# Optimization experiments

Hardware: AMD Instinct MI355X
Metric: run time of the kernel (lower is better)

## Reference

```python
import jax, jax.numpy as jnp
import numpy as np

N = 100_000; E = 1_600_000; G = 64
D_IN = 128; POS = 16; HID = 32; HEADS = 4; OUT = 10
D0 = D_IN + POS; D1 = HID * HEADS
LRELU = 0.2; BN_EPS = 1e-5; DIV_W = 0.1


def setup_inputs() -> dict:
    key = jax.random.key(0)
    k = jax.random.split(key, 24)
    nrm = lambda ki, shape, s: jax.random.normal(ki, shape, dtype=jnp.float32) * s
    inp = {}
    inp["x"] = nrm(k[0], (N, D_IN), 1.0)
    inp["edge_index"] = jax.random.randint(k[1], (2, E), 0, N, dtype=jnp.int32)
    inp["batch"] = jnp.sort(jax.random.randint(k[2], (N,), 0, G, dtype=jnp.int32))
    inp["pos_w"] = nrm(k[3], (2, POS), 0.5)
    inp["pos_b"] = nrm(k[4], (POS,), 0.1)
    inp["w0"] = nrm(k[5], (D0, HEADS * HID), D0 ** -0.5)
    inp["asrc0"] = nrm(k[6], (HEADS, HID), HID ** -0.5)
    inp["adst0"] = nrm(k[7], (HEADS, HID), HID ** -0.5)
    inp["b0"] = nrm(k[8], (D1,), 0.1)
    inp["w1"] = nrm(k[9], (D1, HEADS * HID), D1 ** -0.5)
    inp["asrc1"] = nrm(k[10], (HEADS, HID), HID ** -0.5)
    inp["adst1"] = nrm(k[11], (HEADS, HID), HID ** -0.5)
    inp["b1"] = nrm(k[12], (D1,), 0.1)
    inp["bn_gamma"] = 1.0 + nrm(k[13], (2, D1), 0.1)
    inp["bn_beta"] = nrm(k[14], (2, D1), 0.1)
    inp["bn_mean"] = nrm(k[15], (2, D1), 0.1)
    inp["bn_var"] = jax.random.uniform(k[16], (2, D1), dtype=jnp.float32, minval=0.5, maxval=1.5)
    inp["proj"] = nrm(k[17], (2, HEADS, HID), HID ** -0.5)
    inp["res_w"] = nrm(k[18], (D1, D1), D1 ** -0.5)
    inp["res_b"] = nrm(k[19], (D1,), 0.1)
    inp["task_w"] = nrm(k[20], (D1, OUT), D1 ** -0.5)
    inp["task_b"] = nrm(k[21], (OUT,), 0.1)
    return inp


def _positions(batch):
    # vectorized version of the per-node Python loop: grid layout per graph
    counts = jnp.bincount(batch, length=G)               # nodes per graph
    starts = jnp.cumsum(counts) - counts                  # exclusive cumsum
    local = jnp.arange(N, dtype=counts.dtype) - starts[batch]
    grid = jnp.ceil(jnp.sqrt(counts.astype(jnp.float32))).astype(counts.dtype)
    g = jnp.maximum(grid[batch], 1)
    denom = jnp.maximum(g - 1, 1).astype(jnp.float32)
    row = (local // g).astype(jnp.float32)
    col = (local % g).astype(jnp.float32)
    return jnp.stack([row / denom, col / denom], axis=-1)  # (N, 2)


def _gat(x, src, dst, w, a_src, a_dst, bias):
    # PyG GATConv (v1) with self-loops already appended to src/dst
    n = x.shape[0]
    h = (x @ w).reshape(n, HEADS, HID)                     # (N, H, C)
    e = jax.nn.leaky_relu(jnp.sum(h * a_src, -1)[src] + jnp.sum(h * a_dst, -1)[dst], LRELU)  # (E+N, H)
    m = jax.lax.stop_gradient(jax.ops.segment_max(e, dst, num_segments=n))
    ex = jnp.exp(e - m[dst])
    alpha = ex / jax.ops.segment_sum(ex, dst, num_segments=n)[dst]
    out = jax.ops.segment_sum(alpha[:, :, None] * h[src], dst, num_segments=n)
    return out.reshape(n, D1) + bias


def _div_loss(x, proj):
    # per-head projection, then mean pairwise cosine similarity between heads
    p = x.reshape(-1, HEADS, HID) * proj                   # (N, H, C)
    pn = p / jnp.maximum(jnp.linalg.norm(p, axis=-1, keepdims=True), 1e-8)
    M = jnp.einsum('nhd,ngd->hg', pn, pn) / pn.shape[0]    # mean_n cos(h_i, h_j)
    iu = jnp.triu_indices(HEADS, k=1)
    return jnp.mean(M[iu] ** 2)


def _bn(x, gamma, beta, mean, var):
    return (x - mean) * gamma * jax.lax.rsqrt(var + BN_EPS) + beta


def reference(x, edge_index, batch, pos_w, pos_b, w0, asrc0, adst0, b0,
              w1, asrc1, adst1, b1, bn_gamma, bn_beta, bn_mean, bn_var,
              proj, res_w, res_b, task_w, task_b):
    loops = jnp.arange(N, dtype=edge_index.dtype)
    src = jnp.concatenate([edge_index[0], loops])
    dst = jnp.concatenate([edge_index[1], loops])
    pos = _positions(batch)
    h = jnp.concatenate([x, pos @ pos_w + pos_b], axis=1)  # (N, D0)
    # layer 0
    h = _gat(h, src, dst, w0, asrc0, adst0, b0)
    div = _div_loss(h, proj[0])
    h = jax.nn.elu(_bn(h, bn_gamma[0], bn_beta[0], bn_mean[0], bn_var[0]))
    # layer 1 (+ residual projection of previous activation)
    prev = h
    h = _gat(h, src, dst, w1, asrc1, adst1, b1)
    div = div + _div_loss(h, proj[1])
    h = jax.nn.elu(_bn(h, bn_gamma[1], bn_beta[1], bn_mean[1], bn_var[1]))
    h = h + prev @ res_w + res_b
    # global mean pool over graphs
    counts = jnp.bincount(batch, length=G).astype(h.dtype)
    emb = jax.ops.segment_sum(h, batch, num_segments=G) / jnp.maximum(counts, 1.0)[:, None]
    task = emb @ task_w + task_b
    return task, DIV_W * div, emb
```

## Files before the change

kernel.cpp:

```cpp
#include <hip/hip_runtime.h>
#include <hip/hip_bf16.h>

#define N_NODES 100000
#define N_EDGES 1600000
#define G_GRAPHS 64
#define D_IN 128
#define POS_DIM 16
#define HID 32
#define HEADS 4
#define OUT_DIM 10
#define D0 144
#define D1 128
#define LRELU_SLOPE 0.2f
#define BN_EPS 1e-5f
#define DIV_W 0.1f

#define BK_SHIFT 9
#define BK_NODES 512
#define NB 196
#define TILE_E 4096
#define NTILES ((N_EDGES + TILE_E - 1) / TILE_E)

#define K0P 160

typedef __attribute__((ext_vector_type(8))) short short8v;
typedef __attribute__((ext_vector_type(4))) float f32x4;

__device__ __forceinline__ unsigned short f2b(float f) {
    unsigned u = __float_as_uint(f);
    unsigned r = (u + 0x7FFFu + ((u >> 16) & 1u)) >> 16;
    return (unsigned short)r;
}
__device__ __forceinline__ float blo(unsigned v) { return __uint_as_float(v << 16); }
__device__ __forceinline__ float bhi(unsigned v) { return __uint_as_float(v & 0xFFFF0000u); }

__global__ void k_hist(const int* __restrict__ batch, int* __restrict__ counts, int n) {
    __shared__ int hist[G_GRAPHS];
    if (threadIdx.x < G_GRAPHS) hist[threadIdx.x] = 0;
    __syncthreads();
    for (int i = blockIdx.x * blockDim.x + threadIdx.x; i < n; i += gridDim.x * blockDim.x)
        atomicAdd(&hist[batch[i]], 1);
    __syncthreads();
    if (threadIdx.x < G_GRAPHS) atomicAdd(&counts[threadIdx.x], hist[threadIdx.x]);
}

__global__ void k_gridstats(const int* __restrict__ counts, int* __restrict__ starts,
                            int* __restrict__ gridg) {
    if (threadIdx.x == 0) {
        int run = 0;
        for (int g = 0; g < G_GRAPHS; ++g) {
            starts[g] = run;
            int c = counts[g];
            run += c;
            int s = (int)sqrtf((float)c);
            while ((long long)s * s < c) ++s;
            while (s > 0 && (long long)(s - 1) * (s - 1) >= c) --s;
            gridg[g] = s;
        }
    }
}

__global__ void k_pos(const int* __restrict__ batch, const int* __restrict__ starts,
                      const int* __restrict__ gridg, float2* __restrict__ pos2) {
    int t = blockIdx.x * blockDim.x + threadIdx.x;
    if (t >= N_NODES) return;
    int b = batch[t];
    int local = t - starts[b];
    int g = max(gridg[b], 1);
    float denom = (float)max(g - 1, 1);
    int r = local / g;
    int c = local - r * g;
    pos2[t] = make_float2((float)r / denom, (float)c / denom);
}

__global__ void k_wprep(const float* __restrict__ w0, const float* __restrict__ w1,
                        const float* __restrict__ wr, unsigned short* __restrict__ t0,
                        unsigned short* __restrict__ t1, unsigned short* __restrict__ tr) {
    int t = blockIdx.x * 256 + threadIdx.x;
    if (t < 128 * K0P) {
        int c = t / K0P, k = t % K0P;
        t0[t] = (k < D0) ? f2b(w0[k * 128 + c]) : (unsigned short)0;
    } else if (t < 128 * K0P + 128 * 128) {
        int i = t - 128 * K0P;
        int c = i / 128, k = i % 128;
        t1[i] = f2b(w1[k * 128 + c]);
    } else if (t < 128 * K0P + 2 * 128 * 128) {
        int i = t - 128 * K0P - 128 * 128;
        int c = i / 128, k = i % 128;
        tr[i] = f2b(wr[k * 128 + c]);
    }
}

__global__ void k_bhist(const int* __restrict__ ei, int* __restrict__ bcount) {
    __shared__ int lh[256];
    int tid = threadIdx.x;
    lh[tid] = 0;
    __syncthreads();
    int e = (blockIdx.x * blockDim.x + tid) * 4;
    if (e < N_EDGES) {
        int4 d4 = *reinterpret_cast<const int4*>(ei + N_EDGES + e);
        atomicAdd(&lh[d4.x >> BK_SHIFT], 1);
        atomicAdd(&lh[d4.y >> BK_SHIFT], 1);
        atomicAdd(&lh[d4.z >> BK_SHIFT], 1);
        atomicAdd(&lh[d4.w >> BK_SHIFT], 1);
    }
    __syncthreads();
    if (tid < NB && lh[tid] > 0) atomicAdd(&bcount[tid], lh[tid]);
}

__global__ void k_bscan(const int* __restrict__ bcount, int* __restrict__ bstart,
                        int* __restrict__ bcursor) {
    if (threadIdx.x == 0) {
        int run = 0;
        for (int i = 0; i < NB; ++i) {
            bstart[i] = run;
            bcursor[i] = run;
            run += bcount[i];
        }
        bstart[NB] = run;
    }
}

__global__ __launch_bounds__(256) void k_bucket(const int* __restrict__ ei,
                                                int* __restrict__ bcursor,
                                                int2* __restrict__ pairs) {
    __shared__ int lh[256];
    __shared__ int lstart[256];
    __shared__ int lcur[256];
    __shared__ int gbase[256];
    __shared__ int2 stage[TILE_E];
    const int tid = threadIdx.x;
    const int tile = blockIdx.x * TILE_E;
    const int cnt = min(TILE_E, N_EDGES - tile);
    lh[tid] = 0;
    __syncthreads();
    int sv[16], dv[16];
#pragma unroll
    for (int u = 0; u < 16; ++u) {
        int i = u * 256 + tid;
        if (i < cnt) {
            sv[u] = ei[tile + i];
            dv[u] = ei[N_EDGES + tile + i];
            atomicAdd(&lh[dv[u] >> BK_SHIFT], 1);
        } else {
            sv[u] = -1; dv[u] = -1;
        }
    }
    __syncthreads();
    int own = lh[tid];
    lstart[tid] = own;
    __syncthreads();
    for (int off = 1; off < 256; off <<= 1) {
        int add = (tid >= off) ? lstart[tid - off] : 0;
        __syncthreads();
        lstart[tid] += add;
        __syncthreads();
    }
    int excl = lstart[tid] - own;
    __syncthreads();
    lstart[tid] = excl;
    lcur[tid] = excl;
    __syncthreads();
#pragma unroll
    for (int u = 0; u < 16; ++u) {
        if (dv[u] >= 0) {
            int b = dv[u] >> BK_SHIFT;
            int slot = atomicAdd(&lcur[b], 1);
            stage[slot] = make_int2(sv[u], dv[u]);
        }
    }
    __syncthreads();
    if (tid < NB && own > 0) gbase[tid] = atomicAdd(&bcursor[tid], own);
    __syncthreads();
    for (int i = tid; i < cnt; i += 256) {
        int2 pr = stage[i];
        int b = pr.y >> BK_SHIFT;
        pairs[gbase[b] + (i - lstart[b])] = pr;
    }
}

__global__ __launch_bounds__(256) void k_csr(const int2* __restrict__ pairs,
                                             const int* __restrict__ bstart,
                                             int* __restrict__ offs,
                                             int* __restrict__ csr_src) {
    __shared__ int ldeg[BK_NODES];
    __shared__ int sm[256];
    __shared__ int lcur[BK_NODES];
    const int b = blockIdx.x;
    const int tid = threadIdx.x;
    const int nb0 = b * BK_NODES;
    const int base = bstart[b];
    const int ecnt = bstart[b + 1] - base;
    ldeg[tid] = 0; ldeg[tid + 256] = 0;
    __syncthreads();
    for (int i = tid; i < ecnt; i += 256)
        atomicAdd(&ldeg[pairs[base + i].y - nb0], 1);
    __syncthreads();
    int v0 = ldeg[tid * 2], v1 = ldeg[tid * 2 + 1];
    int tsum = v0 + v1;
    sm[tid] = tsum;
    __syncthreads();
    for (int off = 1; off < 256; off <<= 1) {
        int add = (tid >= off) ? sm[tid - off] : 0;
        __syncthreads();
        sm[tid] += add;
        __syncthreads();
    }
    int excl = sm[tid] - tsum;
    int o0 = base + excl;
    int o1 = o0 + v0;
    lcur[tid * 2] = o0;
    lcur[tid * 2 + 1] = o1;
    int n0 = nb0 + tid * 2, n1 = n0 + 1;
    if (n0 < N_NODES) offs[n0] = o0;
    if (n1 < N_NODES) offs[n1] = o1;
    if (b == NB - 1 && tid == 0) offs[N_NODES] = bstart[NB];
    __syncthreads();
    for (int i = tid; i < ecnt; i += 256) {
        int2 pr = pairs[base + i];
        int pos = atomicAdd(&lcur[pr.y - nb0], 1);
        csr_src[pos] = pr.x;
    }
}

template <int K, int POS, int RES>
__global__ __launch_bounds__(256) void k_gemm3(
        const float* __restrict__ in, const float2* __restrict__ pos2,
        const float* __restrict__ posw, const float* __restrict__ posb,
        const unsigned short* __restrict__ wbT,
        const float* __restrict__ asrc, const float* __restrict__ adst,
        float* __restrict__ es, float* __restrict__ ed,
        unsigned short* __restrict__ outb,
        const unsigned short* __restrict__ wbT2, const float* __restrict__ bias2,
        float* __restrict__ outf2, int n) {
    __shared__ unsigned short At[64 * K];
    const int tid = threadIdx.x;
    const int base = blockIdx.x * 64;
    constexpr int KC4 = K / 4;
    for (int idx = tid; idx < 64 * KC4; idx += 256) {
        int row = idx / KC4, c4 = idx % KC4;
        int grow = base + row;
        float4 v = make_float4(0.f, 0.f, 0.f, 0.f);
        if (grow < n) {
            if (!POS || c4 < 32) {
                v = reinterpret_cast<const float4*>(in)[(size_t)grow * 32 + c4];
            } else if (c4 < 36) {
                float2 p = pos2[grow];
                int q = c4 - 32;
                float4 w0v = reinterpret_cast<const float4*>(posw)[q];
                float4 w1v = reinterpret_cast<const float4*>(posw + POS_DIM)[q];
                float4 bv  = reinterpret_cast<const float4*>(posb)[q];
                v.x = fmaf(p.x, w0v.x, fmaf(p.y, w1v.x, bv.x));
                v.y = fmaf(p.x, w0v.y, fmaf(p.y, w1v.y, bv.y));
                v.z = fmaf(p.x, w0v.z, fmaf(p.y, w1v.z, bv.z));
                v.w = fmaf(p.x, w0v.w, fmaf(p.y, w1v.w, bv.w));
            }
        }
        ushort4 b4;
        b4.x = f2b(v.x); b4.y = f2b(v.y); b4.z = f2b(v.z); b4.w = f2b(v.w);
        unsigned byteoff = (unsigned)((row * K + c4 * 4) * 2) ^ (unsigned)((row & 7) << 4);
        *reinterpret_cast<ushort4*>(reinterpret_cast<char*>(At) + byteoff) = b4;
    }
    __syncthreads();

    const int wv = tid >> 6;
    const int lane = tid & 63;
    const int lrow = lane & 15;
    const int lk8 = lane >> 4;
    f32x4 acc[4][2];
    f32x4 acc2[RES ? 4 : 1][RES ? 2 : 1];
#pragma unroll
    for (int rt = 0; rt < 4; ++rt) {
#pragma unroll
        for (int ct = 0; ct < 2; ++ct) {
            acc[rt][ct] = (f32x4){0.f, 0.f, 0.f, 0.f};
            if (RES) acc2[rt][ct] = (f32x4){0.f, 0.f, 0.f, 0.f};
        }
    }
    const unsigned short* bp0 = wbT + (size_t)(wv * 32 + lrow) * K + lk8 * 8;
    const unsigned short* bp1 = bp0 + 16 * K;
    const unsigned short* cp0 = RES ? (wbT2 + (size_t)(wv * 32 + lrow) * K + lk8 * 8) : nullptr;
    const unsigned short* cp1 = RES ? cp0 + 16 * K : nullptr;

    for (int k0 = 0; k0 < K; k0 += 32) {
        short8v b0 = *reinterpret_cast<const short8v*>(bp0 + k0);
        short8v b1 = *reinterpret_cast<const short8v*>(bp1 + k0);
        short8v a[4];
#pragma unroll
        for (int rt = 0; rt < 4; ++rt) {
            int row = rt * 16 + lrow;
            unsigned byteoff = (unsigned)((row * K + k0 + lk8 * 8) * 2) ^ (unsigned)((row & 7) << 4);
            a[rt] = *reinterpret_cast<const short8v*>(reinterpret_cast<const char*>(At) + byteoff);
        }
#pragma unroll
        for (int rt = 0; rt < 4; ++rt) {
            acc[rt][0] = __builtin_amdgcn_mfma_f32_16x16x32_bf16(a[rt], b0, acc[rt][0], 0, 0, 0);
            acc[rt][1] = __builtin_amdgcn_mfma_f32_16x16x32_bf16(a[rt], b1, acc[rt][1], 0, 0, 0);
        }
        if (RES) {
            short8v c0 = *reinterpret_cast<const short8v*>(cp0 + k0);
            short8v c1 = *reinterpret_cast<const short8v*>(cp1 + k0);
#pragma unroll
            for (int rt = 0; rt < 4; ++rt) {
                acc2[rt][0] = __builtin_amdgcn_mfma_f32_16x16x32_bf16(a[rt], c0, acc2[rt][0], 0, 0, 0);
                acc2[rt][1] = __builtin_amdgcn_mfma_f32_16x16x32_bf16(a[rt], c1, acc2[rt][1], 0, 0, 0);
            }
        }
    }

    float av0 = asrc[wv * 32 + lrow], av1 = asrc[wv * 32 + 16 + lrow];
    float dv0 = adst[wv * 32 + lrow], dv1 = adst[wv * 32 + 16 + lrow];
    float bb0 = 0.f, bb1 = 0.f;
    if (RES) { bb0 = bias2[wv * 32 + lrow]; bb1 = bias2[wv * 32 + 16 + lrow]; }
#pragma unroll
    for (int rt = 0; rt < 4; ++rt) {
#pragma unroll
        for (int r = 0; r < 4; ++r) {
            int row = rt * 16 + lk8 * 4 + r;
            int grow = base + row;
            bool live = (grow < n);
            float v0 = acc[rt][0][r], v1 = acc[rt][1][r];
            if (live) {
                outb[(size_t)grow * 128 + wv * 32 + lrow] = f2b(v0);
                outb[(size_t)grow * 128 + wv * 32 + 16 + lrow] = f2b(v1);
                if (RES) {
                    outf2[(size_t)grow * 128 + wv * 32 + lrow] = acc2[rt][0][r] + bb0;
                    outf2[(size_t)grow * 128 + wv * 32 + 16 + lrow] = acc2[rt][1][r] + bb1;
                }
            }
            float ps = v0 * av0 + v1 * av1;
            float pd = v0 * dv0 + v1 * dv1;
            ps += __shfl_xor(ps, 1); pd += __shfl_xor(pd, 1);
            ps += __shfl_xor(ps, 2); pd += __shfl_xor(pd, 2);
            ps += __shfl_xor(ps, 4); pd += __shfl_xor(pd, 4);
            ps += __shfl_xor(ps, 8); pd += __shfl_xor(pd, 8);
            if (lrow == 0 && live) {
                es[grow * 4 + wv] = ps;
                ed[grow * 4 + wv] = pd;
            }
        }
    }
}

__global__ void k_aggb(const int* __restrict__ csr_src, const int* __restrict__ offs,
                       const float* __restrict__ es, const float* __restrict__ ed,
                       const unsigned* __restrict__ hb32, const float* __restrict__ bias,
                       float* __restrict__ out) {
    int node = blockIdx.x * 4 + (threadIdx.x >> 6);
    if (node >= N_NODES) return;
    int lane = threadIdx.x & 63;
    int hd = lane >> 4;
    float edv = ed[node * 4 + hd];
    int rs = offs[node], re_ = offs[node + 1];
    float ax[4] = {0.f, 0.f, 0.f, 0.f};
    float ay[4] = {0.f, 0.f, 0.f, 0.f};
    float ds[4] = {0.f, 0.f, 0.f, 0.f};
    int j = rs;
    for (; j + 8 <= re_; j += 8) {
        int s[8];
        float e[8];
        unsigned q[8];
#pragma unroll
        for (int u = 0; u < 8; ++u) s[u] = csr_src[j + u];
#pragma unroll
        for (int u = 0; u < 8; ++u) e[u] = es[s[u] * 4 + hd];
#pragma unroll
        for (int u = 0; u < 8; ++u) q[u] = hb32[(size_t)s[u] * 64 + lane];
#pragma unroll
        for (int u = 0; u < 8; ++u) {
            float a = e[u] + edv;
            a = (a > 0.f) ? a : LRELU_SLOPE * a;
            float x = __expf(a);
            ax[u & 3] = fmaf(x, blo(q[u]), ax[u & 3]);
            ay[u & 3] = fmaf(x, bhi(q[u]), ay[u & 3]);
            ds[u & 3] += x;
        }
    }
    for (; j < re_; ++j) {
        int s = csr_src[j];
        float a = es[s * 4 + hd] + edv;
        a = (a > 0.f) ? a : LRELU_SLOPE * a;
        float x = __expf(a);
        unsigned hv = hb32[(size_t)s * 64 + lane];
        ax[0] = fmaf(x, blo(hv), ax[0]);
        ay[0] = fmaf(x, bhi(hv), ay[0]);
        ds[0] += x;
    }
    {
        float a = es[node * 4 + hd] + edv;
        a = (a > 0.f) ? a : LRELU_SLOPE * a;
        float x = __expf(a);
        unsigned hv = hb32[(size_t)node * 64 + lane];
        ax[0] = fmaf(x, blo(hv), ax[0]);
        ay[0] = fmaf(x, bhi(hv), ay[0]);
        ds[0] += x;
    }
    float inv = 1.f / (ds[0] + ds[1] + ds[2] + ds[3]);
    float2 o;
    o.x = fmaf(ax[0] + ax[1] + ax[2] + ax[3], inv, bias[lane * 2]);
    o.y = fmaf(ay[0] + ay[1] + ay[2] + ay[3], inv, bias[lane * 2 + 1]);
    reinterpret_cast<float2*>(out)[(size_t)node * 64 + lane] = o;
}

template <int POOL>
__global__ __launch_bounds__(256) void k_divbn(
        float* __restrict__ h, const float* __restrict__ rbuf,
        const float* __restrict__ proj,
        const float* __restrict__ gamma, const float* __restrict__ beta,
        const float* __restrict__ mean, const float* __restrict__ var,
        float* __restrict__ Msum, const int* __restrict__ batch,
        float* __restrict__ emb) {
    __shared__ float sm[6];
    int tid = threadIdx.x;
    if (tid < 6) sm[tid] = 0.f;
    __syncthreads();
    int lane = tid & 63;
    int wid = tid >> 6;
    const int wave_id = blockIdx.x * 4 + wid;
    const int CH = (N_NODES + 4095) / 4096;
    const int start = wave_id * CH;
    const int end = min(start + CH, N_NODES);
    float2 pj = reinterpret_cast<const float2*>(proj)[lane];
    float2 g2 = reinterpret_cast<const float2*>(gamma)[lane];
    float2 b2 = reinterpret_cast<const float2*>(beta)[lane];
    float2 m2 = reinterpret_cast<const float2*>(mean)[lane];
    float2 v2 = reinterpret_cast<const float2*>(var)[lane];
    float scx = g2.x * rsqrtf(v2.x + BN_EPS);
    float scy = g2.y * rsqrtf(v2.y + BN_EPS);
    float accA = 0.f, accB = 0.f, accC = 0.f;
    float ex = 0.f, ey = 0.f;
    int curg = -1;
    for (int node = start; node < end; ++node) {
        float2 hv = reinterpret_cast<float2*>(h)[(size_t)node * 64 + lane];
        float px = hv.x * pj.x, py = hv.y * pj.y;
        float nn = px * px + py * py;
        nn += __shfl_xor(nn, 1); nn += __shfl_xor(nn, 2);
        nn += __shfl_xor(nn, 4); nn += __shfl_xor(nn, 8);
        float ox = __shfl_xor(px, 16), oy = __shfl_xor(py, 16);
        float d16 = px * ox + py * oy;
        ox = __shfl_xor(px, 32); oy = __shfl_xor(py, 32);
        float d32 = px * ox + py * oy;
        ox = __shfl_xor(px, 48); oy = __shfl_xor(py, 48);
        float d48 = px * ox + py * oy;
        d16 += __shfl_xor(d16, 1); d16 += __shfl_xor(d16, 2);
        d16 += __shfl_xor(d16, 4); d16 += __shfl_xor(d16, 8);
        d32 += __shfl_xor(d32, 1); d32 += __shfl_xor(d32, 2);
        d32 += __shfl_xor(d32, 4); d32 += __shfl_xor(d32, 8);
        d48 += __shfl_xor(d48, 1); d48 += __shfl_xor(d48, 2);
        d48 += __shfl_xor(d48, 4); d48 += __shfl_xor(d48, 8);
        float n_own = fmaxf(sqrtf(nn), 1e-8f);
        float n16 = fmaxf(sqrtf(__shfl_xor(nn, 16)), 1e-8f);
        float n32 = fmaxf(sqrtf(__shfl_xor(nn, 32)), 1e-8f);
        float n48 = fmaxf(sqrtf(__shfl_xor(nn, 48)), 1e-8f);
        accA += d16 / (n_own * n16);
        accB += d32 / (n_own * n32);
        accC += d48 / (n_own * n48);
        float yx = (hv.x - m2.x) * scx + b2.x;
        float yy = (hv.y - m2.y) * scy + b2.y;
        yx = (yx > 0.f) ? yx : (__expf(yx) - 1.f);
        yy = (yy > 0.f) ? yy : (__expf(yy) - 1.f);
        if (rbuf) {
            float2 rb = reinterpret_cast<const float2*>(rbuf)[(size_t)node * 64 + lane];
            yx += rb.x;
            yy += rb.y;
        }
        reinterpret_cast<float2*>(h)[(size_t)node * 64 + lane] = make_float2(yx, yy);
        if (POOL) {
            int g = batch[node];
            if (g != curg) {
                if (curg >= 0) {
                    unsafeAtomicAdd(&emb[curg * 128 + lane * 2], ex);
                    unsafeAtomicAdd(&emb[curg * 128 + lane * 2 + 1], ey);
                }
                curg = g; ex = 0.f; ey = 0.f;
            }
            ex += yx; ey += yy;
        }
    }
    if (POOL && curg >= 0) {
        unsafeAtomicAdd(&emb[curg * 128 + lane * 2], ex);
        unsafeAtomicAdd(&emb[curg * 128 + lane * 2 + 1], ey);
    }
    int g = lane >> 4;
    if ((lane & 15) == 0) {
        if (g == 0) {
            atomicAdd(&sm[0], accA);
            atomicAdd(&sm[1], accB);
            atomicAdd(&sm[2], accC);
        } else if (g == 1) {
            atomicAdd(&sm[4], accB);
            atomicAdd(&sm[3], accC);
        } else if (g == 2) {
            atomicAdd(&sm[5], accA);
        }
    }
    __syncthreads();
    if (tid < 6) unsafeAtomicAdd(&Msum[tid], sm[tid]);
}

__global__ void k_final(const float* __restrict__ emb_ws, const int* __restrict__ counts,
                        const float* __restrict__ task_w, const float* __restrict__ task_b,
                        const float* __restrict__ Msum, float* __restrict__ out) {
    __shared__ float e_lds[G_GRAPHS * 128];
    __shared__ float cnt[G_GRAPHS];
    int tid = threadIdx.x;
    if (tid < G_GRAPHS) cnt[tid] = fmaxf((float)counts[tid], 1.f);
    __syncthreads();
    for (int i = tid; i < G_GRAPHS * 128; i += 256) {
        float v = emb_ws[i] / cnt[i >> 7];
        e_lds[i] = v;
        out[641 + i] = v;
    }
    __syncthreads();
    for (int p = tid; p < G_GRAPHS * OUT_DIM; p += 256) {
        int g = p / OUT_DIM, o = p % OUT_DIM;
        float acc = task_b[o];
#pragma unroll 8
        for (int k = 0; k < 128; ++k) acc = fmaf(e_lds[g * 128 + k], task_w[k * OUT_DIM + o], acc);
        out[p] = acc;
    }
    if (tid == 0) {
        float div = 0.f;
        for (int l = 0; l < 2; ++l) {
            float s = 0.f;
            for (int p = 0; p < 6; ++p) {
                float m = Msum[l * 6 + p] / (float)N_NODES;
                s = fmaf(m, m, s);
            }
            div += s / 6.f;
        }
        out[G_GRAPHS * OUT_DIM] = DIV_W * div;
    }
}

extern "C" void kernel_launch(void* const* d_in, const int* in_sizes, int n_in,
                              void* d_out, int out_size, void* d_ws, size_t ws_size,
                              hipStream_t stream) {
    const float* x      = (const float*)d_in[0];
    const int*   ei     = (const int*)d_in[1];
    const int*   batch  = (const int*)d_in[2];
    const float* pos_w  = (const float*)d_in[3];
    const float* pos_b  = (const float*)d_in[4];
    const float* w0     = (const float*)d_in[5];
    const float* asrc0  = (const float*)d_in[6];
    const float* adst0  = (const float*)d_in[7];
    const float* b0     = (const float*)d_in[8];
    const float* w1     = (const float*)d_in[9];
    const float* asrc1  = (const float*)d_in[10];
    const float* adst1  = (const float*)d_in[11];
    const float* b1     = (const float*)d_in[12];
    const float* bn_gamma = (const float*)d_in[13];
    const float* bn_beta  = (const float*)d_in[14];
    const float* bn_mean  = (const float*)d_in[15];
    const float* bn_var   = (const float*)d_in[16];
    const float* proj   = (const float*)d_in[17];
    const float* res_w  = (const float*)d_in[18];
    const float* res_b  = (const float*)d_in[19];
    const float* task_w = (const float*)d_in[20];
    const float* task_b = (const float*)d_in[21];
    float* out = (float*)d_out;

    unsigned short* wbT0 = (unsigned short*)d_ws;
    unsigned short* wbT1 = wbT0 + 128 * K0P;
    unsigned short* wbTr = wbT1 + 128 * 128;
    float* p = (float*)(wbTr + 128 * 128);
    unsigned short* hb = (unsigned short*)p; p += (size_t)N_NODES * 64;
    float* abuf = p; p += (size_t)N_NODES * D1;
    float* bbuf = p; p += (size_t)N_NODES * D1;
    float* es   = p; p += (size_t)N_NODES * 4;
    float* ed   = p; p += (size_t)N_NODES * 4;
    float2* pos2 = (float2*)p; p += (size_t)N_NODES * 2;
    float* emb  = p; p += G_GRAPHS * 128;
    float* Msum = p; p += 16;
    int* counts = (int*)p;
    int* starts  = counts + G_GRAPHS;
    int* gridg   = starts + G_GRAPHS;
    int* bcount  = gridg + G_GRAPHS;
    int* bstart  = bcount + NB;
    int* bcursor = bstart + NB + 1;
    int* offs    = bcursor + NB;
    int* csr_src = offs + N_NODES + 1;
    int2* pairs  = (int2*)(csr_src + N_EDGES);

    const int B = 256;

    hipMemsetAsync(counts, 0, G_GRAPHS * sizeof(int), stream);
    hipMemsetAsync(Msum, 0, 12 * sizeof(float), stream);
    hipMemsetAsync(bcount, 0, NB * sizeof(int), stream);
    hipMemsetAsync(emb, 0, G_GRAPHS * 128 * sizeof(float), stream);
    k_hist<<<256, B, 0, stream>>>(batch, counts, N_NODES);
    k_gridstats<<<1, 64, 0, stream>>>(counts, starts, gridg);
    k_pos<<<(N_NODES + B - 1) / B, B, 0, stream>>>(batch, starts, gridg, pos2);
    k_wprep<<<(128 * K0P + 2 * 128 * 128 + 255) / 256, 256, 0, stream>>>(
        w0, w1, res_w, wbT0, wbT1, wbTr);

    k_bhist<<<(N_EDGES / 4 + B - 1) / B, B, 0, stream>>>(ei, bcount);
    k_bscan<<<1, 64, 0, stream>>>(bcount, bstart, bcursor);
    k_bucket<<<NTILES, B, 0, stream>>>(ei, bcursor, pairs);
    k_csr<<<NB, B, 0, stream>>>(pairs, bstart, offs, csr_src);

    const int GB = (N_NODES + 63) / 64;

    k_gemm3<K0P, 1, 0><<<GB, 256, 0, stream>>>(
        x, pos2, pos_w, pos_b, wbT0, asrc0, adst0, es, ed, hb,
        nullptr, nullptr, nullptr, N_NODES);
    k_aggb<<<(N_NODES + 3) / 4, B, 0, stream>>>(csr_src, offs, es, ed, (const unsigned*)hb, b0, abuf);
    k_divbn<0><<<1024, B, 0, stream>>>(abuf, nullptr, proj, bn_gamma, bn_beta, bn_mean, bn_var,
                                       Msum, nullptr, nullptr);

    k_gemm3<D1, 0, 1><<<GB, 256, 0, stream>>>(
        abuf, nullptr, nullptr, nullptr, wbT1, asrc1, adst1, es, ed, hb,
        wbTr, res_b, bbuf, N_NODES);
    k_aggb<<<(N_NODES + 3) / 4, B, 0, stream>>>(csr_src, offs, es, ed, (const unsigned*)hb, b1, abuf);
    k_divbn<1><<<1024, B, 0, stream>>>(abuf, bbuf, proj + HEADS * HID, bn_gamma + D1, bn_beta + D1,
                                       bn_mean + D1, bn_var + D1, Msum + 6, batch, emb);

    k_final<<<1, B, 0, stream>>>(emb, counts, task_w, task_b, Msum, out);
}
```

Before: 510.9 us.

## Fuse diversity loss and BN/ELU into aggregation, store intermediates in bf16

The diversity-loss, batch-norm and ELU pass is folded into the attention aggregation kernel, so aggregated features are no longer written and re-read in fp32. The layer-0 activation and the residual projection are now stored as bf16, and the second GEMM loads bf16 inputs directly. Pooling is split into its own small kernel. The edge loop now reads indices with aligned int4 loads over a padded CSR array and masks out-of-range entries instead of using a scalar tail loop. This trades extra per-block atomics and shared-memory syncs for less HBM traffic, and it loses some precision on the intermediates and the residual.

```diff
diff --git a/kernel.cpp b/kernel.cpp
--- a/kernel.cpp
+++ b/kernel.cpp
@@ -223,43 +223,56 @@
     }
 }
 
-template <int K, int POS, int RES>
+template <int K, int POS, int RES, int BF16A>
 __global__ __launch_bounds__(256) void k_gemm3(
-        const float* __restrict__ in, const float2* __restrict__ pos2,
+        const float* __restrict__ in, const unsigned short* __restrict__ inb,
+        const float2* __restrict__ pos2,
         const float* __restrict__ posw, const float* __restrict__ posb,
         const unsigned short* __restrict__ wbT,
         const float* __restrict__ asrc, const float* __restrict__ adst,
         float* __restrict__ es, float* __restrict__ ed,
         unsigned short* __restrict__ outb,
         const unsigned short* __restrict__ wbT2, const float* __restrict__ bias2,
-        float* __restrict__ outf2, int n) {
+        unsigned short* __restrict__ outb2, int n) {
     __shared__ unsigned short At[64 * K];
     const int tid = threadIdx.x;
     const int base = blockIdx.x * 64;
-    constexpr int KC4 = K / 4;
-    for (int idx = tid; idx < 64 * KC4; idx += 256) {
-        int row = idx / KC4, c4 = idx % KC4;
-        int grow = base + row;
-        float4 v = make_float4(0.f, 0.f, 0.f, 0.f);
-        if (grow < n) {
-            if (!POS || c4 < 32) {
-                v = reinterpret_cast<const float4*>(in)[(size_t)grow * 32 + c4];
-            } else if (c4 < 36) {
-                float2 p = pos2[grow];
-                int q = c4 - 32;
-                float4 w0v = reinterpret_cast<const float4*>(posw)[q];
-                float4 w1v = reinterpret_cast<const float4*>(posw + POS_DIM)[q];
-                float4 bv  = reinterpret_cast<const float4*>(posb)[q];
-                v.x = fmaf(p.x, w0v.x, fmaf(p.y, w1v.x, bv.x));
-                v.y = fmaf(p.x, w0v.y, fmaf(p.y, w1v.y, bv.y));
-                v.z = fmaf(p.x, w0v.z, fmaf(p.y, w1v.z, bv.z));
-                v.w = fmaf(p.x, w0v.w, fmaf(p.y, w1v.w, bv.w));
+    if (BF16A) {
+        constexpr int KC8 = K / 8;
+        for (int idx = tid; idx < 64 * KC8; idx += 256) {
+            int row = idx / KC8, g = idx % KC8;
+            int grow = base + row;
+            short8v v = (short8v)(short)0;
+            if (grow < n) v = *reinterpret_cast<const short8v*>(inb + (size_t)grow * 128 + g * 8);
+            unsigned byteoff = (unsigned)((row * K + g * 8) * 2) ^ (unsigned)((row & 7) << 4);
+            *reinterpret_cast<short8v*>(reinterpret_cast<char*>(At) + byteoff) = v;
+        }
+    } else {
+        constexpr int KC4 = K / 4;
+        for (int idx = tid; idx < 64 * KC4; idx += 256) {
+            int row = idx / KC4, c4 = idx % KC4;
+            int grow = base + row;
+            float4 v = make_float4(0.f, 0.f, 0.f, 0.f);
+            if (grow < n) {
+                if (!POS || c4 < 32) {
+                    v = reinterpret_cast<const float4*>(in)[(size_t)grow * 32 + c4];
+                } else if (c4 < 36) {
+                    float2 p = pos2[grow];
+                    int q = c4 - 32;
+                    float4 w0v = reinterpret_cast<const float4*>(posw)[q];
+                    float4 w1v = reinterpret_cast<const float4*>(posw + POS_DIM)[q];
+                    float4 bv  = reinterpret_cast<const float4*>(posb)[q];
+                    v.x = fmaf(p.x, w0v.x, fmaf(p.y, w1v.x, bv.x));
+                    v.y = fmaf(p.x, w0v.y, fmaf(p.y, w1v.y, bv.y));
+                    v.z = fmaf(p.x, w0v.z, fmaf(p.y, w1v.z, bv.z));
+                    v.w = fmaf(p.x, w0v.w, fmaf(p.y, w1v.w, bv.w));
+                }
             }
-        }
-        ushort4 b4;
-        b4.x = f2b(v.x); b4.y = f2b(v.y); b4.z = f2b(v.z); b4.w = f2b(v.w);
-        unsigned byteoff = (unsigned)((row * K + c4 * 4) * 2) ^ (unsigned)((row & 7) << 4);
-        *reinterpret_cast<ushort4*>(reinterpret_cast<char*>(At) + byteoff) = b4;
+            ushort4 b4;
+            b4.x = f2b(v.x); b4.y = f2b(v.y); b4.z = f2b(v.z); b4.w = f2b(v.w);
+            unsigned byteoff = (unsigned)((row * K + c4 * 4) * 2) ^ (unsigned)((row & 7) << 4);
+            *reinterpret_cast<ushort4*>(reinterpret_cast<char*>(At) + byteoff) = b4;
+        }
     }
     __syncthreads();
 
@@ -324,8 +337,8 @@
                 outb[(size_t)grow * 128 + wv * 32 + lrow] = f2b(v0);
                 outb[(size_t)grow * 128 + wv * 32 + 16 + lrow] = f2b(v1);
                 if (RES) {
-                    outf2[(size_t)grow * 128 + wv * 32 + lrow] = acc2[rt][0][r] + bb0;
-                    outf2[(size_t)grow * 128 + wv * 32 + 16 + lrow] = acc2[rt][1][r] + bb1;
+                    outb2[(size_t)grow * 128 + wv * 32 + lrow] = f2b(acc2[rt][0][r] + bb0);
+                    outb2[(size_t)grow * 128 + wv * 32 + 16 + lrow] = f2b(acc2[rt][1][r] + bb1);
                 }
             }
             float ps = v0 * av0 + v1 * av1;
@@ -342,51 +355,52 @@
     }
 }
 
-__global__ void k_aggb(const int* __restrict__ csr_src, const int* __restrict__ offs,
-                       const float* __restrict__ es, const float* __restrict__ ed,
-                       const unsigned* __restrict__ hb32, const float* __restrict__ bias,
-                       float* __restrict__ out) {
-    int node = blockIdx.x * 4 + (threadIdx.x >> 6);
-    if (node >= N_NODES) return;
-    int lane = threadIdx.x & 63;
-    int hd = lane >> 4;
-    float edv = ed[node * 4 + hd];
-    int rs = offs[node], re_ = offs[node + 1];
+template <int LAYER>
+__global__ __launch_bounds__(256) void k_aggf(
+        const int* __restrict__ csr_src, const int* __restrict__ offs,
+        const float* __restrict__ es, const float* __restrict__ ed,
+        const unsigned* __restrict__ hb32, const float* __restrict__ bias,
+        const float* __restrict__ proj, const float* __restrict__ gamma,
+        const float* __restrict__ beta, const float* __restrict__ mean,
+        const float* __restrict__ var, float* __restrict__ Msum,
+        const unsigned* __restrict__ rbuf16, unsigned* __restrict__ outb16,
+        float* __restrict__ outf) {
+    __shared__ float smp[6];
+    const int tid = threadIdx.x;
+    if (tid < 6) smp[tid] = 0.f;
+    __syncthreads();
+    const int node = blockIdx.x * 4 + (tid >> 6);
+    const bool live = (node < N_NODES);
+    const int lane = tid & 63;
+    const int hd = lane >> 4;
+    float edv = live ? ed[node * 4 + hd] : 0.f;
+    int rs = 0, re_ = 0;
+    if (live) { rs = offs[node]; re_ = offs[node + 1]; }
     float ax[4] = {0.f, 0.f, 0.f, 0.f};
     float ay[4] = {0.f, 0.f, 0.f, 0.f};
     float ds[4] = {0.f, 0.f, 0.f, 0.f};
-    int j = rs;
-    for (; j + 8 <= re_; j += 8) {
-        int s[8];
+    for (int j = rs & ~7; j < re_; j += 8) {
+        int4 c0 = *reinterpret_cast<const int4*>(csr_src + j);
+        int4 c1 = *reinterpret_cast<const int4*>(csr_src + j + 4);
+        int s[8] = {c0.x, c0.y, c0.z, c0.w, c1.x, c1.y, c1.z, c1.w};
         float e[8];
         unsigned q[8];
 #pragma unroll
-        for (int u = 0; u < 8; ++u) s[u] = csr_src[j + u];
-#pragma unroll
         for (int u = 0; u < 8; ++u) e[u] = es[s[u] * 4 + hd];
 #pragma unroll
         for (int u = 0; u < 8; ++u) q[u] = hb32[(size_t)s[u] * 64 + lane];
 #pragma unroll
         for (int u = 0; u < 8; ++u) {
+            int idx = j + u;
             float a = e[u] + edv;
             a = (a > 0.f) ? a : LRELU_SLOPE * a;
-            float x = __expf(a);
+            float x = (idx >= rs && idx < re_) ? __expf(a) : 0.f;
             ax[u & 3] = fmaf(x, blo(q[u]), ax[u & 3]);
             ay[u & 3] = fmaf(x, bhi(q[u]), ay[u & 3]);
             ds[u & 3] += x;
         }
     }
-    for (; j < re_; ++j) {
-        int s = csr_src[j];
-        float a = es[s * 4 + hd] + edv;
-        a = (a > 0.f) ? a : LRELU_SLOPE * a;
-        float x = __expf(a);
-        unsigned hv = hb32[(size_t)s * 64 + lane];
-        ax[0] = fmaf(x, blo(hv), ax[0]);
-        ay[0] = fmaf(x, bhi(hv), ay[0]);
-        ds[0] += x;
-    }
-    {
+    if (live) {
         float a = es[node * 4 + hd] + edv;
         a = (a > 0.f) ? a : LRELU_SLOPE * a;
         float x = __expf(a);
@@ -395,107 +409,98 @@
         ay[0] = fmaf(x, bhi(hv), ay[0]);
         ds[0] += x;
     }
-    float inv = 1.f / (ds[0] + ds[1] + ds[2] + ds[3]);
-    float2 o;
-    o.x = fmaf(ax[0] + ax[1] + ax[2] + ax[3], inv, bias[lane * 2]);
-    o.y = fmaf(ay[0] + ay[1] + ay[2] + ay[3], inv, bias[lane * 2 + 1]);
-    reinterpret_cast<float2*>(out)[(size_t)node * 64 + lane] = o;
-}
-
-template <int POOL>
-__global__ __launch_bounds__(256) void k_divbn(
-        float* __restrict__ h, const float* __restrict__ rbuf,
-        const float* __restrict__ proj,
-        const float* __restrict__ gamma, const float* __restrict__ beta,
-        const float* __restrict__ mean, const float* __restrict__ var,
-        float* __restrict__ Msum, const int* __restrict__ batch,
-        float* __restrict__ emb) {
-    __shared__ float sm[6];
-    int tid = threadIdx.x;
-    if (tid < 6) sm[tid] = 0.f;
-    __syncthreads();
-    int lane = tid & 63;
-    int wid = tid >> 6;
+    float inv = live ? (1.f / (ds[0] + ds[1] + ds[2] + ds[3])) : 0.f;
+    float ox_ = fmaf(ax[0] + ax[1] + ax[2] + ax[3], inv, live ? bias[lane * 2] : 0.f);
+    float oy_ = fmaf(ay[0] + ay[1] + ay[2] + ay[3], inv, live ? bias[lane * 2 + 1] : 0.f);
+
+    float2 pj = reinterpret_cast<const float2*>(proj)[lane];
+    float px = ox_ * pj.x, py = oy_ * pj.y;
+    float nn = px * px + py * py;
+    nn += __shfl_xor(nn, 1); nn += __shfl_xor(nn, 2);
+    nn += __shfl_xor(nn, 4); nn += __shfl_xor(nn, 8);
+    float tx = __shfl_xor(px, 16), ty = __shfl_xor(py, 16);
+    float d16 = px * tx + py * ty;
+    tx = __shfl_xor(px, 32); ty = __shfl_xor(py, 32);
+    float d32 = px * tx + py * ty;
+    tx = __shfl_xor(px, 48); ty = __shfl_xor(py, 48);
+    float d48 = px * tx + py * ty;
+    d16 += __shfl_xor(d16, 1); d16 += __shfl_xor(d16, 2);
+    d16 += __shfl_xor(d16, 4); d16 += __shfl_xor(d16, 8);
+    d32 += __shfl_xor(d32, 1); d32 += __shfl_xor(d32, 2);
+    d32 += __shfl_xor(d32, 4); d32 += __shfl_xor(d32, 8);
+    d48 += __shfl_xor(d48, 1); d48 += __shfl_xor(d48, 2);
+    d48 += __shfl_xor(d48, 4); d48 += __shfl_xor(d48, 8);
+    float n_own = fmaxf(sqrtf(nn), 1e-8f);
+    float n16 = fmaxf(sqrtf(__shfl_xor(nn, 16)), 1e-8f);
+    float n32 = fmaxf(sqrtf(__shfl_xor(nn, 32)), 1e-8f);
+    float n48 = fmaxf(sqrtf(__shfl_xor(nn, 48)), 1e-8f);
+    float accA = live ? d16 / (n_own * n16) : 0.f;
+    float accB = live ? d32 / (n_own * n32) : 0.f;
+    float accC = live ? d48 / (n_own * n48) : 0.f;
+
+    float2 g2 = reinterpret_cast<const float2*>(gamma)[lane];
+    float2 b2 = reinterpret_cast<const float2*>(beta)[lane];
+    float2 m2 = reinterpret_cast<const float2*>(mean)[lane];
+    float2 v2 = reinterpret_cast<const float2*>(var)[lane];
+    float yx = (ox_ - m2.x) * g2.x * rsqrtf(v2.x + BN_EPS) + b2.x;
+    float yy = (oy_ - m2.y) * g2.y * rsqrtf(v2.y + BN_EPS) + b2.y;
+    yx = (yx > 0.f) ? yx : (__expf(yx) - 1.f);
+    yy = (yy > 0.f) ? yy : (__expf(yy) - 1.f);
+    if (live) {
+        if (LAYER == 1) {
+            unsigned rb = rbuf16[(size_t)node * 64 + lane];
+            yx += blo(rb);
+            yy += bhi(rb);
+            reinterpret_cast<float2*>(outf)[(size_t)node * 64 + lane] = make_float2(yx, yy);
+        } else {
+            outb16[(size_t)node * 64 + lane] = (unsigned)f2b(yx) | ((unsigned)f2b(yy) << 16);
+        }
+    }
+    int g = lane >> 4;
+    if ((lane & 15) == 0) {
+        if (g == 0) {
+            atomicAdd(&smp[0], accA);
+            atomicAdd(&smp[1], accB);
+            atomicAdd(&smp[2], accC);
+        } else if (g == 1) {
+            atomicAdd(&smp[4], accB);
+            atomicAdd(&smp[3], accC);
+        } else if (g == 2) {
+            atomicAdd(&smp[5], accA);
+        }
+    }
+    __syncthreads();
+    if (tid < 6) unsafeAtomicAdd(&Msum[tid], smp[tid]);
+}
+
+__global__ __launch_bounds__(256) void k_pool2(const float* __restrict__ h,
+                                               const int* __restrict__ batch,
+                                               float* __restrict__ emb) {
+    const int tid = threadIdx.x;
+    const int lane = tid & 63;
+    const int wid = tid >> 6;
     const int wave_id = blockIdx.x * 4 + wid;
     const int CH = (N_NODES + 4095) / 4096;
     const int start = wave_id * CH;
     const int end = min(start + CH, N_NODES);
-    float2 pj = reinterpret_cast<const float2*>(proj)[lane];
-    float2 g2 = reinterpret_cast<const float2*>(gamma)[lane];
-    float2 b2 = reinterpret_cast<const float2*>(beta)[lane];
-    float2 m2 = reinterpret_cast<const float2*>(mean)[lane];
-    float2 v2 = reinterpret_cast<const float2*>(var)[lane];
-    float scx = g2.x * rsqrtf(v2.x + BN_EPS);
-    float scy = g2.y * rsqrtf(v2.y + BN_EPS);
-    float accA = 0.f, accB = 0.f, accC = 0.f;
     float ex = 0.f, ey = 0.f;
     int curg = -1;
     for (int node = start; node < end; ++node) {
-        float2 hv = reinterpret_cast<float2*>(h)[(size_t)node * 64 + lane];
-        float px = hv.x * pj.x, py = hv.y * pj.y;
-        float nn = px * px + py * py;
-        nn += __shfl_xor(nn, 1); nn += __shfl_xor(nn, 2);
-        nn += __shfl_xor(nn, 4); nn += __shfl_xor(nn, 8);
-        float ox = __shfl_xor(px, 16), oy = __shfl_xor(py, 16);
-        float d16 = px * ox + py * oy;
-        ox = __shfl_xor(px, 32); oy = __shfl_xor(py, 32);
-        float d32 = px * ox + py * oy;
-        ox = __shfl_xor(px, 48); oy = __shfl_xor(py, 48);
-        float d48 = px * ox + py * oy;
-        d16 += __shfl_xor(d16, 1); d16 += __shfl_xor(d16, 2);
-        d16 += __shfl_xor(d16, 4); d16 += __shfl_xor(d16, 8);
-        d32 += __shfl_xor(d32, 1); d32 += __shfl_xor(d32, 2);
-        d32 += __shfl_xor(d32, 4); d32 += __shfl_xor(d32, 8);
-        d48 += __shfl_xor(d48, 1); d48 += __shfl_xor(d48, 2);
-        d48 += __shfl_xor(d48, 4); d48 += __shfl_xor(d48, 8);
-        float n_own = fmaxf(sqrtf(nn), 1e-8f);
-        float n16 = fmaxf(sqrtf(__shfl_xor(nn, 16)), 1e-8f);
-        float n32 = fmaxf(sqrtf(__shfl_xor(nn, 32)), 1e-8f);
-        float n48 = fmaxf(sqrtf(__shfl_xor(nn, 48)), 1e-8f);
-        accA += d16 / (n_own * n16);
-        accB += d32 / (n_own * n32);
-        accC += d48 / (n_own * n48);
-        float yx = (hv.x - m2.x) * scx + b2.x;
-        float yy = (hv.y - m2.y) * scy + b2.y;
-        yx = (yx > 0.f) ? yx : (__expf(yx) - 1.f);
-        yy = (yy > 0.f) ? yy : (__expf(yy) - 1.f);
-        if (rbuf) {
-            float2 rb = reinterpret_cast<const float2*>(rbuf)[(size_t)node * 64 + lane];
-            yx += rb.x;
-            yy += rb.y;
-        }
-        reinterpret_cast<float2*>(h)[(size_t)node * 64 + lane] = make_float2(yx, yy);
-        if (POOL) {
-            int g = batch[node];
-            if (g != curg) {
-                if (curg >= 0) {
-                    unsafeAtomicAdd(&emb[curg * 128 + lane * 2], ex);
-                    unsafeAtomicAdd(&emb[curg * 128 + lane * 2 + 1], ey);
-                }
-                curg = g; ex = 0.f; ey = 0.f;
+        float2 hv = reinterpret_cast<const float2*>(h)[(size_t)node * 64 + lane];
+        int g = batch[node];
+        if (g != curg) {
+            if (curg >= 0) {
+                unsafeAtomicAdd(&emb[curg * 128 + lane * 2], ex);
+                unsafeAtomicAdd(&emb[curg * 128 + lane * 2 + 1], ey);
             }
-            ex += yx; ey += yy;
-        }
-    }
-    if (POOL && curg >= 0) {
+            curg = g; ex = 0.f; ey = 0.f;
+        }
+        ex += hv.x; ey += hv.y;
+    }
+    if (curg >= 0) {
         unsafeAtomicAdd(&emb[curg * 128 + lane * 2], ex);
         unsafeAtomicAdd(&emb[curg * 128 + lane * 2 + 1], ey);
     }
-    int g = lane >> 4;
-    if ((lane & 15) == 0) {
-        if (g == 0) {
-            atomicAdd(&sm[0], accA);
-            atomicAdd(&sm[1], accB);
-            atomicAdd(&sm[2], accC);
-        } else if (g == 1) {
-            atomicAdd(&sm[4], accB);
-            atomicAdd(&sm[3], accC);
-        } else if (g == 2) {
-            atomicAdd(&sm[5], accA);
-        }
-    }
-    __syncthreads();
-    if (tid < 6) unsafeAtomicAdd(&Msum[tid], sm[tid]);
 }
 
 __global__ void k_final(const float* __restrict__ emb_ws, const int* __restrict__ counts,
@@ -563,10 +568,11 @@
     unsigned short* wbT0 = (unsigned short*)d_ws;
     unsigned short* wbT1 = wbT0 + 128 * K0P;
     unsigned short* wbTr = wbT1 + 128 * 128;
-    float* p = (float*)(wbTr + 128 * 128);
-    unsigned short* hb = (unsigned short*)p; p += (size_t)N_NODES * 64;
+    unsigned short* hb   = wbTr + 128 * 128;
+    unsigned short* hb0  = hb + (size_t)N_NODES * 128;
+    unsigned short* bbuf = hb0 + (size_t)N_NODES * 128;
+    float* p = (float*)(bbuf + (size_t)N_NODES * 128);
     float* abuf = p; p += (size_t)N_NODES * D1;
-    float* bbuf = p; p += (size_t)N_NODES * D1;
     float* es   = p; p += (size_t)N_NODES * 4;
     float* ed   = p; p += (size_t)N_NODES * 4;
     float2* pos2 = (float2*)p; p += (size_t)N_NODES * 2;
@@ -579,8 +585,8 @@
     int* bstart  = bcount + NB;
     int* bcursor = bstart + NB + 1;
     int* offs    = bcursor + NB;
-    int* csr_src = offs + N_NODES + 1;
-    int2* pairs  = (int2*)(csr_src + N_EDGES);
+    int* csr_src = (int*)(((uintptr_t)(offs + N_NODES + 1) + 15) & ~(uintptr_t)15);
+    int2* pairs  = (int2*)(csr_src + N_EDGES + 8);
 
     const int B = 256;
 
@@ -588,6 +594,7 @@
     hipMemsetAsync(Msum, 0, 12 * sizeof(float), stream);
     hipMemsetAsync(bcount, 0, NB * sizeof(int), stream);
     hipMemsetAsync(emb, 0, G_GRAPHS * 128 * sizeof(float), stream);
+    hipMemsetAsync(csr_src + N_EDGES, 0, 8 * sizeof(int), stream);
     k_hist<<<256, B, 0, stream>>>(batch, counts, N_NODES);
     k_gridstats<<<1, 64, 0, stream>>>(counts, starts, gridg);
     k_pos<<<(N_NODES + B - 1) / B, B, 0, stream>>>(batch, starts, gridg, pos2);
@@ -600,20 +607,24 @@
     k_csr<<<NB, B, 0, stream>>>(pairs, bstart, offs, csr_src);
 
     const int GB = (N_NODES + 63) / 64;
-
-    k_gemm3<K0P, 1, 0><<<GB, 256, 0, stream>>>(
-        x, pos2, pos_w, pos_b, wbT0, asrc0, adst0, es, ed, hb,
+    const int AB = (N_NODES + 3) / 4;
+
+    k_gemm3<K0P, 1, 0, 0><<<GB, 256, 0, stream>>>(
+        x, nullptr, pos2, pos_w, pos_b, wbT0, asrc0, adst0, es, ed, hb,
         nullptr, nullptr, nullptr, N_NODES);
-    k_aggb<<<(N_NODES + 3) / 4, B, 0, stream>>>(csr_src, offs, es, ed, (const unsigned*)hb, b0, abuf);
-    k_divbn<0><<<1024, B, 0, stream>>>(abuf, nullptr, proj, bn_gamma, bn_beta, bn_mean, bn_var,
-                                       Msum, nullptr, nullptr);
-
-    k_gemm3<D1, 0, 1><<<GB, 256, 0, stream>>>(
-        abuf, nullptr, nullptr, nullptr, wbT1, asrc1, adst1, es, ed, hb,
+    k_aggf<0><<<AB, B, 0, stream>>>(
+        csr_src, offs, es, ed, (const unsigned*)hb, b0, proj,
+        bn_gamma, bn_beta, bn_mean, bn_var, Msum,
+        nullptr, (unsigned*)hb0, nullptr);
+
+    k_gemm3<D1, 0, 1, 1><<<GB, 256, 0, stream>>>(
+        nullptr, hb0, nullptr, nullptr, nullptr, wbT1, asrc1, adst1, es, ed, hb,
         wbTr, res_b, bbuf, N_NODES);
-    k_aggb<<<(N_NODES + 3) / 4, B, 0, stream>>>(csr_src, offs, es, ed, (const unsigned*)hb, b1, abuf);
-    k_divbn<1><<<1024, B, 0, stream>>>(abuf, bbuf, proj + HEADS * HID, bn_gamma + D1, bn_beta + D1,
-                                       bn_mean + D1, bn_var + D1, Msum + 6, batch, emb);
-
+    k_aggf<1><<<AB, B, 0, stream>>>(
+        csr_src, offs, es, ed, (const unsigned*)hb, b1, proj + HEADS * HID,
+        bn_gamma + D1, bn_beta + D1, bn_mean + D1, bn_var + D1, Msum + 6,
+        (const unsigned*)bbuf, nullptr, abuf);
+
+    k_pool2<<<1024, B, 0, stream>>>(abuf, batch, emb);
     k_final<<<1, B, 0, stream>>>(emb, counts, task_w, task_b, Msum, out);
 }
```

Result: slower. 890.1 us (+74.2%).
